# Optimization experiments

Hardware: AMD Instinct MI355X
Metric: run time of the kernel (lower is better)

The kernel has to match this reference:

```python
import jax, jax.numpy as jnp
import numpy as np

B, T, F = 32, 1024, 512
EPS = 1e-6


def setup_inputs() -> dict:
    key = jax.random.key(0)
    k1, k2, k3 = jax.random.split(key, 3)
    x = jax.random.normal(k1, (B, T, F), dtype=jnp.float32)
    aggr_w = jax.random.normal(k2, (F, 1), dtype=jnp.float32) / np.sqrt(F).astype(np.float32)
    aggr_b = jnp.zeros((1,), dtype=jnp.float32)
    seq_len = jax.random.randint(k3, (B,), T // 2, T + 1, dtype=jnp.int32).at[0].set(T)
    return {"x": x, "aggr_w": aggr_w, "aggr_b": aggr_b, "seq_len": seq_len}


def reference(x, aggr_w, aggr_b, seq_len):
    # --- gate weights: sigmoid(Linear(F->1)) ---
    w = jax.nn.sigmoid(jnp.einsum('btf,fo->bto', x, aggr_w) + aggr_b)  # [B,T,1]
    ws = w[..., 0]                                                      # [B,T]

    # --- valley detection (comparisons on detached neighbors; non-diff anyway) ---
    wd = jax.lax.stop_gradient(ws)
    sb = jnp.pad(wd[:, :-1], ((0, 0), (1, 0)))  # previous frame, 0 at t=0
    sa = jnp.pad(wd[:, 1:], ((0, 0), (0, 1)))   # next frame, 0 at t=T-1
    valley = (wd < sb) & (wd < sa)              # [B,T] bool

    start_mask = valley.at[:, 0].set(True)
    end_mask = valley.at[:, 0].set(False).at[:, -1].set(True)
    counts = jnp.sum(start_mask, axis=1)        # segments per batch (== end count)

    # sorted valley positions per batch (pad value T pushes pads to the end)
    idx = jnp.arange(T, dtype=jnp.int32)
    starts = jnp.sort(jnp.where(start_mask, idx, T), axis=1)            # [B,T]
    ends = jnp.minimum(jnp.sort(jnp.where(end_mask, idx, T), axis=1) + 2, T)

    # statically pad max_counts -> T; torch zero-fills unused segment rows
    seg_ids = jnp.arange(T, dtype=jnp.int32)
    valid = seg_ids[None, :] < counts[:, None]                          # [B,S]
    seg_start = jnp.where(valid, starts, 0)
    seg_end = jnp.where(valid, ends, 0)

    # segment indicator == utri[end] - utri[start]  (1 for start <= t < end)
    t = jnp.arange(T, dtype=jnp.int32)
    seg_mask = ((t[None, None, :] >= seg_start[:, :, None]) &
                (t[None, None, :] < seg_end[:, :, None])).astype(x.dtype)  # [B,S,T]

    # segment-weighted mean (dense bmm like torch)
    alpha_h = ws[..., None] * x                                         # [B,T,F]
    num = jnp.einsum('bst,btf->bsf', seg_mask, alpha_h)                 # [B,S,F]
    den = jnp.maximum(jnp.einsum('bst,bt->bs', seg_mask, ws), EPS)      # [B,S]
    out = num / den[..., None]                                          # [B,S,F]

    # new sequence mask (torch uses dynamic x.shape[1] == max(counts))
    lengths = seq_len.astype(jnp.float32)
    max_counts = jnp.max(counts).astype(jnp.float32)
    new_lengths = (lengths / lengths[0] * max_counts).astype(jnp.int32)  # [B]
    new_mask = seg_ids[None, :] < new_lengths[:, None]                   # [B,S]
    return out, new_mask
```

## Files before the change

kernel.cpp:

```cpp
#include <hip/hip_runtime.h>

#define TT 1024
#define FF 512
#define BB 32
#define MAXSEG 513

typedef float f32x4 __attribute__((ext_vector_type(4)));

__device__ __forceinline__ void nt_store4(float* p, f32x4 v) {
    __builtin_nontemporal_store(v, (f32x4*)p);
}

__global__ __launch_bounds__(256) void gate_kernel(const float* __restrict__ x,
                                                   const float* __restrict__ w,
                                                   const float* __restrict__ bias,
                                                   float* __restrict__ ws) {
    int wid  = threadIdx.x >> 6;
    int lane = threadIdx.x & 63;
    int row  = blockIdx.x * 4 + wid;
    const float4* xr = (const float4*)(x + (size_t)row * FF);
    const float4* wr = (const float4*)w;
    float4 x0 = xr[lane * 2],     x1 = xr[lane * 2 + 1];
    float4 w0 = wr[lane * 2],     w1 = wr[lane * 2 + 1];
    double acc = (double)x0.x * w0.x + (double)x0.y * w0.y +
                 (double)x0.z * w0.z + (double)x0.w * w0.w +
                 (double)x1.x * w1.x + (double)x1.y * w1.y +
                 (double)x1.z * w1.z + (double)x1.w * w1.w;
    #pragma unroll
    for (int off = 32; off; off >>= 1) acc += __shfl_down(acc, off);
    if (lane == 0) {
        float z = (float)acc + bias[0];
        ws[row] = 1.0f / (1.0f + expf(-z));
    }
}

__global__ __launch_bounds__(1024) void seg_kernel(const float* __restrict__ ws,
                                                   int* __restrict__ seg_start,
                                                   int* __restrict__ seg_end,
                                                   float* __restrict__ den,
                                                   int* __restrict__ counts) {
    int b = blockIdx.x, t = threadIdx.x;
    __shared__ float w[TT];
    __shared__ float p[TT];
    __shared__ unsigned long long words[16];
    __shared__ float wavesum[16];
    __shared__ int sst[MAXSEG];
    __shared__ int sen[MAXSEG];

    w[t] = ws[b * TT + t];
    __syncthreads();

    float wt = w[t];
    bool valley = (t > 0) && (t < TT - 1) && (wt < w[t - 1]) && (wt < w[t + 1]);
    unsigned long long m = __ballot(valley);
    int wid = t >> 6, lane = t & 63;
    if (lane == 0) words[wid] = m;

    float s = wt;
    #pragma unroll
    for (int off = 1; off < 64; off <<= 1) {
        float v = __shfl_up(s, off);
        if (lane >= off) s += v;
    }
    if (lane == 63) wavesum[wid] = s;
    __syncthreads();

    float offset = 0.0f;
    for (int i = 0; i < wid; ++i) offset += wavesum[i];
    p[t] = s + offset;

    int before = __popcll(m & ((1ull << lane) - 1ull));
    int total = 0;
    for (int i = 0; i < 16; ++i) {
        int pc = __popcll(words[i]);
        if (i < wid) before += pc;
        total += pc;
    }
    if (valley) {
        int en = t + 2; if (en > TT) en = TT;
        sst[before + 1] = t;
        sen[before]     = en;
    }
    if (t == 0) {
        sst[0]     = 0;
        sen[total] = TT;
        counts[b]  = total + 1;
    }
    __syncthreads();

    int cnt = total + 1;
    if (t < cnt) {
        int st = sst[t], en = sen[t];
        seg_start[b * TT + t] = st;
        seg_end  [b * TT + t] = en;
        float d = p[en - 1] - (st > 0 ? p[st - 1] : 0.0f);
        den[b * TT + t] = fmaxf(d, 1e-6f);
    }
}

__global__ __launch_bounds__(256) void out_kernel(const float* __restrict__ x,
                                                  const float* __restrict__ ws,
                                                  const int* __restrict__ seg_start,
                                                  const int* __restrict__ seg_end,
                                                  const float* __restrict__ den,
                                                  const int* __restrict__ counts,
                                                  const int* __restrict__ seq,
                                                  float* __restrict__ out) {
    int bid = blockIdx.x;

    if ((bid & 255) == 0) {
        int bb = bid >> 8;
        int maxc = 0;
        #pragma unroll
        for (int i = 0; i < BB; ++i) maxc = max(maxc, counts[i]);
        float l0 = (float)seq[0];
        float v  = ((float)seq[bb] / l0) * (float)maxc;
        int nl = (int)v;
        float* mrow = out + (size_t)BB * TT * FF + (size_t)bb * TT;
        int s4 = threadIdx.x * 4;
        f32x4 mv;
        mv.x = (s4 + 0 < nl) ? 1.0f : 0.0f;
        mv.y = (s4 + 1 < nl) ? 1.0f : 0.0f;
        mv.z = (s4 + 2 < nl) ? 1.0f : 0.0f;
        mv.w = (s4 + 3 < nl) ? 1.0f : 0.0f;
        nt_store4(mrow + s4, mv);
    }

    int swz = (bid & 7) * (BB * TT / 4 / 8) + (bid >> 3);

    int wid  = threadIdx.x >> 6;
    int lane = threadIdx.x & 63;
    int bs = swz * 4 + wid;
    int b  = bs >> 10;
    int s  = bs & 1023;
    float* orow = out + (size_t)bs * FF + lane * 8;
    if (s >= counts[b]) {
        f32x4 z = 0.0f;
        nt_store4(orow, z);
        nt_store4(orow + 4, z);
        return;
    }
    int st = seg_start[bs], en = seg_end[bs];
    float inv = 1.0f / den[bs];
    const float* xb  = x + (size_t)b * TT * FF + lane * 8;
    const float* wsr = ws + b * TT;
    f32x4 a0 = 0.0f, a1 = 0.0f;
    #pragma unroll
    for (int k = 0; k < 8; ++k) {
        int t  = st + k;
        int tc = t < en ? t : en - 1;
        float wt = t < en ? wsr[tc] : 0.0f;
        const f32x4* xr = (const f32x4*)(xb + (size_t)tc * FF);
        a0 += wt * xr[0];
        a1 += wt * xr[1];
    }
    for (int t = st + 8; t < en; ++t) {
        float wt = wsr[t];
        const f32x4* xr = (const f32x4*)(xb + (size_t)t * FF);
        a0 += wt * xr[0];
        a1 += wt * xr[1];
    }
    nt_store4(orow,     a0 * inv);
    nt_store4(orow + 4, a1 * inv);
}

extern "C" void kernel_launch(void* const* d_in, const int* in_sizes, int n_in,
                              void* d_out, int out_size, void* d_ws, size_t ws_size,
                              hipStream_t stream) {
    const float* x    = (const float*)d_in[0];
    const float* aw   = (const float*)d_in[1];
    const float* ab   = (const float*)d_in[2];
    const int*   seq  = (const int*)d_in[3];
    float* out = (float*)d_out;

    float* ws     = (float*)d_ws;
    float* den    = ws + BB * TT;
    int*   sstart = (int*)(ws + 2 * BB * TT);
    int*   send   = (int*)(ws + 3 * BB * TT);
    int*   counts = (int*)(ws + 4 * BB * TT);

    gate_kernel<<<BB * TT / 4, 256, 0, stream>>>(x, aw, ab, ws);
    seg_kernel<<<BB, 1024, 0, stream>>>(ws, sstart, send, den, counts);
    out_kernel<<<BB * TT / 4, 256, 0, stream>>>(x, ws, sstart, send, den, counts,
                                                seq, out);
}
```

Baseline: 40.34 us.

## Move zero-fill of upper segment rows into gate kernel, halve output grid

At most 512 segments can exist per batch, because valleys can never be adjacent. So output rows 512..1023 are always zero. Their zero stores now run inside the gate kernel, interleaved one block in three with the gate's dot-product blocks. The aim is to overlap the write-only traffic of the zero-fill with the read-heavy gate pass. The output kernel then launches half as many blocks and covers only segment rows 0..511. The gate kernel gains extra blocks and mixes read and write streams, and the result relies on the structural bound on segment count.

```diff
diff --git a/kernel.cpp b/kernel.cpp
--- a/kernel.cpp
+++ b/kernel.cpp
@@ -11,13 +11,28 @@
     __builtin_nontemporal_store(v, (f32x4*)p);
 }
 
-__global__ __launch_bounds__(256) void gate_kernel(const float* __restrict__ x,
-                                                   const float* __restrict__ w,
-                                                   const float* __restrict__ bias,
-                                                   float* __restrict__ ws) {
+__global__ __launch_bounds__(256) void gate_zfill_kernel(const float* __restrict__ x,
+                                                         const float* __restrict__ w,
+                                                         const float* __restrict__ bias,
+                                                         float* __restrict__ ws,
+                                                         float* __restrict__ out) {
+    unsigned bid = blockIdx.x;
+    unsigned q = bid / 3u, r = bid - 3u * q;
     int wid  = threadIdx.x >> 6;
     int lane = threadIdx.x & 63;
-    int row  = blockIdx.x * 4 + wid;
+
+    if (r == 2u) {
+        int rr = (int)q * 4 + wid;
+        int b  = rr >> 9;
+        int s  = 512 + (rr & 511);
+        float* orow = out + ((size_t)b * TT + s) * FF + lane * 8;
+        f32x4 z = 0.0f;
+        nt_store4(orow, z);
+        nt_store4(orow + 4, z);
+        return;
+    }
+
+    int row = (int)(2u * q + r) * 4 + wid;
     const float4* xr = (const float4*)(x + (size_t)row * FF);
     const float4* wr = (const float4*)w;
     float4 x0 = xr[lane * 2],     x1 = xr[lane * 2 + 1];
@@ -108,8 +123,8 @@
                                                   float* __restrict__ out) {
     int bid = blockIdx.x;
 
-    if ((bid & 255) == 0) {
-        int bb = bid >> 8;
+    if ((bid & 127) == 0) {
+        int bb = bid >> 7;
         int maxc = 0;
         #pragma unroll
         for (int i = 0; i < BB; ++i) maxc = max(maxc, counts[i]);
@@ -126,13 +141,14 @@
         nt_store4(mrow + s4, mv);
     }
 
-    int swz = (bid & 7) * (BB * TT / 4 / 8) + (bid >> 3);
+    int swz = (bid & 7) * 512 + (bid >> 3);
 
     int wid  = threadIdx.x >> 6;
     int lane = threadIdx.x & 63;
-    int bs = swz * 4 + wid;
-    int b  = bs >> 10;
-    int s  = bs & 1023;
+    int rr = swz * 4 + wid;
+    int b  = rr >> 9;
+    int s  = rr & 511;
+    int bs = b * TT + s;
     float* orow = out + (size_t)bs * FF + lane * 8;
     if (s >= counts[b]) {
         f32x4 z = 0.0f;
@@ -179,8 +195,8 @@
     int*   send   = (int*)(ws + 3 * BB * TT);
     int*   counts = (int*)(ws + 4 * BB * TT);
 
-    gate_kernel<<<BB * TT / 4, 256, 0, stream>>>(x, aw, ab, ws);
+    gate_zfill_kernel<<<12288, 256, 0, stream>>>(x, aw, ab, ws, out);
     seg_kernel<<<BB, 1024, 0, stream>>>(ws, sstart, send, den, counts);
-    out_kernel<<<BB * TT / 4, 256, 0, stream>>>(x, ws, sstart, send, den, counts,
-                                                seq, out);
-}
+    out_kernel<<<4096, 256, 0, stream>>>(x, ws, sstart, send, den, counts,
+                                         seq, out);
+}
```

Result: slower. 41.56 us (+3.0%).

## Process groups of four consecutive segments per wavefront sharing overlapping rows

Applied to the files above, without the earlier changes.

Each wavefront now handles four consecutive segments and streams x rows once across their combined span, emitting each segment when its end is reached. Consecutive segments overlap by one frame (end = next valley + 2), so the carry of the previous row lets the next segment's accumulator start without reloading. This cuts the redundant x reads and the per-segment index loads, and it quarters the grid. The cost is fewer waves in flight, plus a serial scan per wave whose length depends on how long the segments are, which can create load imbalance.

```diff
diff --git a/kernel.cpp b/kernel.cpp
--- a/kernel.cpp
+++ b/kernel.cpp
@@ -4,6 +4,8 @@
 #define FF 512
 #define BB 32
 #define MAXSEG 513
+#define GRP 4
+#define GPB (TT / GRP)
 
 typedef float f32x4 __attribute__((ext_vector_type(4)));
 
@@ -108,8 +110,8 @@
                                                   float* __restrict__ out) {
     int bid = blockIdx.x;
 
-    if ((bid & 255) == 0) {
-        int bb = bid >> 8;
+    if ((bid & 63) == 0) {
+        int bb = bid >> 6;
         int maxc = 0;
         #pragma unroll
         for (int i = 0; i < BB; ++i) maxc = max(maxc, counts[i]);
@@ -126,42 +128,78 @@
         nt_store4(mrow + s4, mv);
     }
 
-    int swz = (bid & 7) * (BB * TT / 4 / 8) + (bid >> 3);
-
+    int swz = (bid & 7) * 256 + (bid >> 3);
     int wid  = threadIdx.x >> 6;
     int lane = threadIdx.x & 63;
-    int bs = swz * 4 + wid;
-    int b  = bs >> 10;
-    int s  = bs & 1023;
-    float* orow = out + (size_t)bs * FF + lane * 8;
-    if (s >= counts[b]) {
-        f32x4 z = 0.0f;
-        nt_store4(orow, z);
-        nt_store4(orow + 4, z);
-        return;
-    }
-    int st = seg_start[bs], en = seg_end[bs];
-    float inv = 1.0f / den[bs];
-    const float* xb  = x + (size_t)b * TT * FF + lane * 8;
-    const float* wsr = ws + b * TT;
+    int gid = swz * 4 + wid;
+    int b   = gid >> 8;
+    int g   = gid & (GPB - 1);
+    int cnt = counts[b];
+    int sA  = g * GRP;
+    float* obase = out + ((size_t)b * TT + sA) * FF + lane * 8;
+
+    int live = cnt - sA;
+    if (live > GRP) live = GRP;
+    if (live < 0)  live = 0;
+    f32x4 z = 0.0f;
+    for (int k = live; k < GRP; ++k) {
+        nt_store4(obase + (size_t)k * FF,     z);
+        nt_store4(obase + (size_t)k * FF + 4, z);
+    }
+    if (live == 0) return;
+
+    int sEnd = sA + live;
+    const int*   sstB = seg_start + b * TT;
+    const int*   senB = seg_end   + b * TT;
+    const float* denB = den       + b * TT;
+    const float* wsr  = ws        + b * TT;
+    const float* xb   = x + (size_t)b * TT * FF + lane * 8;
+
+    int curSeg = sA;
+    int curEnd = senB[curSeg];
+    int t0 = sstB[sA];
+    int t1 = senB[sEnd - 1];
+
     f32x4 a0 = 0.0f, a1 = 0.0f;
-    #pragma unroll
-    for (int k = 0; k < 8; ++k) {
-        int t  = st + k;
-        int tc = t < en ? t : en - 1;
-        float wt = t < en ? wsr[tc] : 0.0f;
-        const f32x4* xr = (const f32x4*)(xb + (size_t)tc * FF);
-        a0 += wt * xr[0];
-        a1 += wt * xr[1];
-    }
-    for (int t = st + 8; t < en; ++t) {
-        float wt = wsr[t];
-        const f32x4* xr = (const f32x4*)(xb + (size_t)t * FF);
-        a0 += wt * xr[0];
-        a1 += wt * xr[1];
-    }
-    nt_store4(orow,     a0 * inv);
-    nt_store4(orow + 4, a1 * inv);
+    f32x4 p0 = 0.0f, p1 = 0.0f;
+    float wp = 0.0f;
+
+    for (int t = t0; t < t1; t += 4) {
+        int ta = t;
+        int tb = (t + 1 < t1) ? t + 1 : t1 - 1;
+        int tc = (t + 2 < t1) ? t + 2 : t1 - 1;
+        int td = (t + 3 < t1) ? t + 3 : t1 - 1;
+        const f32x4* qa = (const f32x4*)(xb + (size_t)ta * FF);
+        const f32x4* qb = (const f32x4*)(xb + (size_t)tb * FF);
+        const f32x4* qc = (const f32x4*)(xb + (size_t)tc * FF);
+        const f32x4* qd = (const f32x4*)(xb + (size_t)td * FF);
+        f32x4 ra0 = qa[0], ra1 = qa[1];
+        f32x4 rb0 = qb[0], rb1 = qb[1];
+        f32x4 rc0 = qc[0], rc1 = qc[1];
+        f32x4 rd0 = qd[0], rd1 = qd[1];
+
+        #pragma unroll
+        for (int k = 0; k < 4; ++k) {
+            int tk = t + k;
+            if (tk >= t1) break;
+            f32x4 r0 = (k == 0) ? ra0 : (k == 1) ? rb0 : (k == 2) ? rc0 : rd0;
+            f32x4 r1 = (k == 0) ? ra1 : (k == 1) ? rb1 : (k == 2) ? rc1 : rd1;
+            float wv = wsr[tk];
+            a0 += wv * r0;
+            a1 += wv * r1;
+            while (tk == curEnd - 1) {
+                float inv = 1.0f / denB[curSeg];
+                nt_store4(obase + (size_t)(curSeg - sA) * FF,     a0 * inv);
+                nt_store4(obase + (size_t)(curSeg - sA) * FF + 4, a1 * inv);
+                ++curSeg;
+                if (curSeg >= sEnd) { curEnd = 0x7fffffff; break; }
+                a0 = wp * p0 + wv * r0;
+                a1 = wp * p1 + wv * r1;
+                curEnd = senB[curSeg];
+            }
+            p0 = r0; p1 = r1; wp = wv;
+        }
+    }
 }
 
 extern "C" void kernel_launch(void* const* d_in, const int* in_sizes, int n_in,
@@ -181,6 +219,6 @@
 
     gate_kernel<<<BB * TT / 4, 256, 0, stream>>>(x, aw, ab, ws);
     seg_kernel<<<BB, 1024, 0, stream>>>(ws, sstart, send, den, counts);
-    out_kernel<<<BB * TT / 4, 256, 0, stream>>>(x, ws, sstart, send, den, counts,
-                                                seq, out);
-}
+    out_kernel<<<2048, 256, 0, stream>>>(x, ws, sstart, send, den, counts,
+                                         seq, out);
+}
```

After: 47.63 us. +18.1%, slower.

## Fuse segment detection into output kernel, recomputing valleys per block

Applied to the files above, without the earlier changes.

Removes the separate single-block-per-batch segmentation kernel and recomputes valley detection, prefix sums and segment bounds redundantly inside every output block from the gate weights held in shared memory. Blocks whose segment range starts at or past 512 skip the scan and write zeros directly, relying on the segment count never exceeding 513. Mask rows move to 32 extra blocks that each recount valleys across all batches. This drops one launch and the global round-trip of segment metadata, at the cost of redundant per-block scan work and a serial 32-batch loop in the mask blocks.

```diff
diff --git a/kernel.cpp b/kernel.cpp
--- a/kernel.cpp
+++ b/kernel.cpp
@@ -3,7 +3,6 @@
 #define TT 1024
 #define FF 512
 #define BB 32
-#define MAXSEG 513
 
 typedef float f32x4 __attribute__((ext_vector_type(4)));
 
@@ -34,153 +33,156 @@
     }
 }
 
-__global__ __launch_bounds__(1024) void seg_kernel(const float* __restrict__ ws,
-                                                   int* __restrict__ seg_start,
-                                                   int* __restrict__ seg_end,
-                                                   float* __restrict__ den,
-                                                   int* __restrict__ counts) {
-    int b = blockIdx.x, t = threadIdx.x;
-    __shared__ float w[TT];
-    __shared__ float p[TT];
-    __shared__ unsigned long long words[16];
-    __shared__ float wavesum[16];
-    __shared__ int sst[MAXSEG];
-    __shared__ int sen[MAXSEG];
+__global__ __launch_bounds__(256) void out_fused(const float* __restrict__ x,
+                                                 const float* __restrict__ ws,
+                                                 const int* __restrict__ seq,
+                                                 float* __restrict__ out) {
+    int bid   = blockIdx.x;
+    int tid   = threadIdx.x;
+    int wavid = tid >> 6;
+    int lane  = tid & 63;
 
-    w[t] = ws[b * TT + t];
-    __syncthreads();
+    __shared__ float wsh[TT];
+    __shared__ float psm[TT];
+    __shared__ int   sval[512];
+    __shared__ int   wsi[4];
+    __shared__ float wsf[4];
+    __shared__ float wrow[TT];
+    __shared__ int   redc[4];
 
-    float wt = w[t];
-    bool valley = (t > 0) && (t < TT - 1) && (wt < w[t - 1]) && (wt < w[t + 1]);
-    unsigned long long m = __ballot(valley);
-    int wid = t >> 6, lane = t & 63;
-    if (lane == 0) words[wid] = m;
-
-    float s = wt;
-    #pragma unroll
-    for (int off = 1; off < 64; off <<= 1) {
-        float v = __shfl_up(s, off);
-        if (lane >= off) s += v;
-    }
-    if (lane == 63) wavesum[wid] = s;
-    __syncthreads();
-
-    float offset = 0.0f;
-    for (int i = 0; i < wid; ++i) offset += wavesum[i];
-    p[t] = s + offset;
-
-    int before = __popcll(m & ((1ull << lane) - 1ull));
-    int total = 0;
-    for (int i = 0; i < 16; ++i) {
-        int pc = __popcll(words[i]);
-        if (i < wid) before += pc;
-        total += pc;
-    }
-    if (valley) {
-        int en = t + 2; if (en > TT) en = TT;
-        sst[before + 1] = t;
-        sen[before]     = en;
-    }
-    if (t == 0) {
-        sst[0]     = 0;
-        sen[total] = TT;
-        counts[b]  = total + 1;
-    }
-    __syncthreads();
-
-    int cnt = total + 1;
-    if (t < cnt) {
-        int st = sst[t], en = sen[t];
-        seg_start[b * TT + t] = st;
-        seg_end  [b * TT + t] = en;
-        float d = p[en - 1] - (st > 0 ? p[st - 1] : 0.0f);
-        den[b * TT + t] = fmaxf(d, 1e-6f);
-    }
-}
-
-__global__ __launch_bounds__(256) void out_kernel(const float* __restrict__ x,
-                                                  const float* __restrict__ ws,
-                                                  const int* __restrict__ seg_start,
-                                                  const int* __restrict__ seg_end,
-                                                  const float* __restrict__ den,
-                                                  const int* __restrict__ counts,
-                                                  const int* __restrict__ seq,
-                                                  float* __restrict__ out) {
-    int bid = blockIdx.x;
-
-    if ((bid & 255) == 0) {
-        int bb = bid >> 8;
+    if (bid >= 8192) {
+        int bb = bid - 8192;
         int maxc = 0;
-        #pragma unroll
-        for (int i = 0; i < BB; ++i) maxc = max(maxc, counts[i]);
+        for (int b2 = 0; b2 < BB; ++b2) {
+            ((f32x4*)wrow)[tid] = ((const f32x4*)(ws + b2 * TT))[tid];
+            __syncthreads();
+            int c = 0;
+            #pragma unroll
+            for (int k = 0; k < 4; ++k) {
+                int t = tid * 4 + k;
+                if (t > 0 && t < TT - 1) {
+                    float w = wrow[t];
+                    c += (w < wrow[t - 1] && w < wrow[t + 1]) ? 1 : 0;
+                }
+            }
+            #pragma unroll
+            for (int off = 32; off; off >>= 1) c += __shfl_down(c, off);
+            if (lane == 0) redc[wavid] = c;
+            __syncthreads();
+            int cnt = redc[0] + redc[1] + redc[2] + redc[3] + 1;
+            maxc = max(maxc, cnt);
+        }
         float l0 = (float)seq[0];
         float v  = ((float)seq[bb] / l0) * (float)maxc;
         int nl = (int)v;
         float* mrow = out + (size_t)BB * TT * FF + (size_t)bb * TT;
-        int s4 = threadIdx.x * 4;
+        int s4 = tid * 4;
         f32x4 mv;
         mv.x = (s4 + 0 < nl) ? 1.0f : 0.0f;
         mv.y = (s4 + 1 < nl) ? 1.0f : 0.0f;
         mv.z = (s4 + 2 < nl) ? 1.0f : 0.0f;
         mv.w = (s4 + 3 < nl) ? 1.0f : 0.0f;
         nt_store4(mrow + s4, mv);
+        return;
     }
 
-    int swz = (bid & 7) * (BB * TT / 4 / 8) + (bid >> 3);
+    int swz = (bid & 7) * 1024 + (bid >> 3);
+    int bs  = swz * 4 + wavid;
+    int b   = bs >> 10;
+    int s   = bs & 1023;
+    float* orow = out + (size_t)bs * FF + lane * 8;
+    int qs = (swz * 4) & 1023;
 
-    int wid  = threadIdx.x >> 6;
-    int lane = threadIdx.x & 63;
-    int bs = swz * 4 + wid;
-    int b  = bs >> 10;
-    int s  = bs & 1023;
-    float* orow = out + (size_t)bs * FF + lane * 8;
-    if (s >= counts[b]) {
+    if (qs >= 512) {
         f32x4 z = 0.0f;
         nt_store4(orow, z);
         nt_store4(orow + 4, z);
         return;
     }
-    int st = seg_start[bs], en = seg_end[bs];
-    float inv = 1.0f / den[bs];
-    const float* xb  = x + (size_t)b * TT * FF + lane * 8;
+
     const float* wsr = ws + b * TT;
-    f32x4 a0 = 0.0f, a1 = 0.0f;
+    f32x4 w4 = ((const f32x4*)wsr)[tid];
+    ((f32x4*)wsh)[tid] = w4;
+    __syncthreads();
+
+    int t0 = tid * 4;
+    unsigned flags = 0; int nv = 0;
     #pragma unroll
-    for (int k = 0; k < 8; ++k) {
-        int t  = st + k;
-        int tc = t < en ? t : en - 1;
-        float wt = t < en ? wsr[tc] : 0.0f;
-        const f32x4* xr = (const f32x4*)(xb + (size_t)tc * FF);
-        a0 += wt * xr[0];
-        a1 += wt * xr[1];
+    for (int k = 0; k < 4; ++k) {
+        int t = t0 + k;
+        bool vly = false;
+        if (t > 0 && t < TT - 1) {
+            float w = wsh[t];
+            vly = (w < wsh[t - 1]) && (w < wsh[t + 1]);
+        }
+        flags |= (vly ? 1u : 0u) << k;
+        nv += vly ? 1 : 0;
     }
-    for (int t = st + 8; t < en; ++t) {
-        float wt = wsr[t];
-        const f32x4* xr = (const f32x4*)(xb + (size_t)t * FF);
-        a0 += wt * xr[0];
-        a1 += wt * xr[1];
+    float ts = w4.x + w4.y + w4.z + w4.w;
+    int iscan = nv; float fscan = ts;
+    #pragma unroll
+    for (int off = 1; off < 64; off <<= 1) {
+        int   vi = __shfl_up(iscan, off);
+        float vf = __shfl_up(fscan, off);
+        if (lane >= off) { iscan += vi; fscan += vf; }
     }
-    nt_store4(orow,     a0 * inv);
-    nt_store4(orow + 4, a1 * inv);
+    if (lane == 63) { wsi[wavid] = iscan; wsf[wavid] = fscan; }
+    __syncthreads();
+    int ibase = 0; float fbase = 0.0f;
+    for (int w2 = 0; w2 < wavid; ++w2) { ibase += wsi[w2]; fbase += wsf[w2]; }
+    int   r   = ibase + iscan - nv;
+    float run = fbase + fscan - ts;
+    #pragma unroll
+    for (int k = 0; k < 4; ++k)
+        if ((flags >> k) & 1u) sval[r++] = t0 + k;
+    #pragma unroll
+    for (int k = 0; k < 4; ++k) { run += wsh[t0 + k]; psm[t0 + k] = run; }
+    __syncthreads();
+    int totv = wsi[0] + wsi[1] + wsi[2] + wsi[3];
+    int cnt  = totv + 1;
+
+    if (s < cnt) {
+        int st = (s == 0)    ? 0  : sval[s - 1];
+        int en = (s == totv) ? TT : (sval[s] + 2);
+        float d   = psm[en - 1] - (st > 0 ? psm[st - 1] : 0.0f);
+        float inv = 1.0f / fmaxf(d, 1e-6f);
+        const float* xb = x + (size_t)b * TT * FF + lane * 8;
+        f32x4 a0 = 0.0f, a1 = 0.0f;
+        #pragma unroll
+        for (int k = 0; k < 8; ++k) {
+            int t  = st + k;
+            int tc = t < en ? t : en - 1;
+            float wt = t < en ? wsh[tc] : 0.0f;
+            const f32x4* xr = (const f32x4*)(xb + (size_t)tc * FF);
+            a0 += wt * xr[0];
+            a1 += wt * xr[1];
+        }
+        for (int t = st + 8; t < en; ++t) {
+            float wt = wsh[t];
+            const f32x4* xr = (const f32x4*)(xb + (size_t)t * FF);
+            a0 += wt * xr[0];
+            a1 += wt * xr[1];
+        }
+        nt_store4(orow,     a0 * inv);
+        nt_store4(orow + 4, a1 * inv);
+    } else {
+        f32x4 z = 0.0f;
+        nt_store4(orow, z);
+        nt_store4(orow + 4, z);
+    }
 }
 
 extern "C" void kernel_launch(void* const* d_in, const int* in_sizes, int n_in,
                               void* d_out, int out_size, void* d_ws, size_t ws_size,
                               hipStream_t stream) {
-    const float* x    = (const float*)d_in[0];
-    const float* aw   = (const float*)d_in[1];
-    const float* ab   = (const float*)d_in[2];
-    const int*   seq  = (const int*)d_in[3];
+    const float* x   = (const float*)d_in[0];
+    const float* aw  = (const float*)d_in[1];
+    const float* ab  = (const float*)d_in[2];
+    const int*   seq = (const int*)d_in[3];
     float* out = (float*)d_out;
 
-    float* ws     = (float*)d_ws;
-    float* den    = ws + BB * TT;
-    int*   sstart = (int*)(ws + 2 * BB * TT);
-    int*   send   = (int*)(ws + 3 * BB * TT);
-    int*   counts = (int*)(ws + 4 * BB * TT);
+    float* ws = (float*)d_ws;
 
     gate_kernel<<<BB * TT / 4, 256, 0, stream>>>(x, aw, ab, ws);
-    seg_kernel<<<BB, 1024, 0, stream>>>(ws, sstart, send, den, counts);
-    out_kernel<<<BB * TT / 4, 256, 0, stream>>>(x, ws, sstart, send, den, counts,
-                                                seq, out);
+    out_fused<<<8192 + 32, 256, 0, stream>>>(x, ws, seq, out);
 }
```

After: 65.52 us. +62.4%, slower.
